# Kernel optimization log

Measured on AMD Instinct MI355X. Metric: run time of the kernel, lower is better.

Reference implementation:

```python
import jax, jax.numpy as jnp
import numpy as np

NUM_EMBEDDINGS = 512
EMBEDDING_DIM = 64
COMMITMENT_COST = 0.25


def setup_inputs() -> dict:
    key = jax.random.key(0)
    k1, k2 = jax.random.split(key)
    inputs = jax.random.normal(k1, (16, EMBEDDING_DIM, 4096), dtype=jnp.float32)
    # torch init: uniform(-1/num_embeddings, 1/num_embeddings)
    codebook = jax.random.uniform(
        k2, (NUM_EMBEDDINGS, EMBEDDING_DIM), dtype=jnp.float32,
        minval=-1.0 / NUM_EMBEDDINGS, maxval=1.0 / NUM_EMBEDDINGS)
    return {"inputs": inputs, "codebook": codebook}


def reference(inputs, codebook):
    # inputs: [B, D, T] -> permute to [B, T, D]
    x = jnp.transpose(inputs, (0, 2, 1))
    B, T, D = x.shape
    K = codebook.shape[0]
    flat = x.reshape(-1, D)  # [N, D]

    distances = (jnp.sum(flat * flat, axis=1, keepdims=True)
                 + jnp.sum(codebook * codebook, axis=1)
                 - 2.0 * flat @ codebook.T)  # [N, K]
    idx = jnp.argmin(distances, axis=1)  # [N]
    encodings = jax.nn.one_hot(idx, K, dtype=jnp.float32)  # [N, K]

    # direct gather == encodings @ codebook
    quantized = codebook[idx].reshape(B, T, D)

    e_latent_loss = jnp.mean((jax.lax.stop_gradient(quantized) - x) ** 2)
    q_latent_loss = jnp.mean((quantized - jax.lax.stop_gradient(x)) ** 2)
    loss = q_latent_loss + COMMITMENT_COST * e_latent_loss

    # straight-through estimator
    quantized_st = x + jax.lax.stop_gradient(quantized - x)

    avg_probs = jnp.mean(encodings, axis=0)
    perplexity = jnp.exp(-jnp.sum(avg_probs * jnp.log(avg_probs + 1e-10)))

    return (loss, jnp.transpose(quantized_st, (0, 2, 1)), perplexity, encodings)
```

## Files before the change

### kernel.cpp

```cpp
#include <hip/hip_runtime.h>

#define B_ 16
#define D_ 64
#define T_ 4096
#define K_ 512
#define N_ (B_*T_)
#define Q_ (B_*D_*T_)
#define ENC_OFF ((size_t)(2 + Q_))

#define WS_LOSS    0
#define WS_HIST    16
#define WS_NE      2064
#define WS_CBH     4608
#define WS_CBL     70144

typedef __bf16 bf16x8 __attribute__((ext_vector_type(8)));
typedef float  f32x4  __attribute__((ext_vector_type(4)));
typedef float  f32x2  __attribute__((ext_vector_type(2)));

__global__ __launch_bounds__(256) void k0_init(const float* __restrict__ cb,
                                               float* __restrict__ ne,
                                               int* __restrict__ hist,
                                               double* __restrict__ loss,
                                               bf16x8* __restrict__ cbh,
                                               bf16x8* __restrict__ cbl) {
    int bidx = blockIdx.x, tid = threadIdx.x;

    {
        int code = bidx * 32 + (tid >> 3), sl = tid & 7;
        float s = 0.f;
#pragma unroll
        for (int j = 0; j < 8; ++j) { float c = cb[code * 64 + sl * 8 + j]; s = fmaf(c, c, s); }
        s += __shfl_xor(s, 1); s += __shfl_xor(s, 2); s += __shfl_xor(s, 4);
        if (sl == 0) ne[code] = s;
    }
    if (bidx == 0) {
        hist[tid] = 0; hist[tid + 256] = 0;
        if (tid == 0) *loss = 0.0;
    }

    int e = bidx * 256 + tid;
    int ct = e >> 7, ks = (e >> 6) & 1, lane = e & 63;
    int code  = ct * 16 + (lane & 15);
    int dbase = ks * 32 + ((lane >> 4) << 3);
    bf16x8 h, l;
#pragma unroll
    for (int j = 0; j < 8; ++j) {
        float v = cb[code * 64 + dbase + j];
        __bf16 hv = (__bf16)v;
        __bf16 lv = (__bf16)(v - (float)hv);
        h[j] = hv; l[j] = lv;
    }
    cbh[(ct * 2 + ks) * 64 + lane] = h;
    cbl[(ct * 2 + ks) * 64 + lane] = l;
}

__global__ __launch_bounds__(256, 8) void k_main(const float* __restrict__ in,
                                                 const float* __restrict__ cb,
                                                 const bf16x8* __restrict__ cbh,
                                                 const bf16x8* __restrict__ cbl,
                                                 const float* __restrict__ ne,
                                                 float* __restrict__ out,
                                                 f32x2* __restrict__ enc2,
                                                 int* __restrict__ hist,
                                                 double* __restrict__ loss) {
    __shared__ float X[64][33];
    __shared__ float ne_s[512];
    __shared__ float smin[2][32];
    __shared__ int   smid[2][32];
    __shared__ int   sidx[32];
    int tid = threadIdx.x;
    int n0 = blockIdx.x * 32;
    int b  = n0 >> 12, t0 = n0 & (T_ - 1);

    {
        int d = tid >> 2, c0 = (tid & 3) * 8;
        const float4* ip = (const float4*)(in + ((size_t)b * 64 + d) * T_ + t0 + c0);
        float4 v0 = ip[0], v1 = ip[1];
        X[d][c0 + 0] = v0.x; X[d][c0 + 1] = v0.y; X[d][c0 + 2] = v0.z; X[d][c0 + 3] = v0.w;
        X[d][c0 + 4] = v1.x; X[d][c0 + 5] = v1.y; X[d][c0 + 6] = v1.z; X[d][c0 + 7] = v1.w;
    }
    ne_s[tid] = ne[tid];
    ne_s[tid + 256] = ne[tid + 256];
    __syncthreads();

    int w = tid >> 6, lane = tid & 63;
    int col = lane & 15, q = lane >> 4;
    int rt = w & 1;
    int ch = w >> 1;

    bf16x8 Ah[2], Al[2];
#pragma unroll
    for (int ks = 0; ks < 2; ++ks) {
        bf16x8 h, l;
#pragma unroll
        for (int j = 0; j < 8; ++j) {
            float v = X[ks * 32 + q * 8 + j][rt * 16 + col];
            __bf16 hv = (__bf16)v;
            __bf16 lv = (__bf16)(v - (float)hv);
            h[j] = hv; l[j] = lv;
        }
        Ah[ks] = h; Al[ks] = l;
    }

    float m1[4]; int i1[4];
#pragma unroll
    for (int e = 0; e < 4; ++e) { m1[e] = 3.4e38f; i1[e] = 0; }

    for (int c16 = 0; c16 < 16; ++c16) {
        int ct = ch * 16 + c16;
        bf16x8 Bh0 = cbh[(ct * 2 + 0) * 64 + lane];
        bf16x8 Bh1 = cbh[(ct * 2 + 1) * 64 + lane];
        bf16x8 Bl0 = cbl[(ct * 2 + 0) * 64 + lane];
        bf16x8 Bl1 = cbl[(ct * 2 + 1) * 64 + lane];
        float nev = ne_s[ct * 16 + col];
        int code = ct * 16 + col;
        f32x4 acc = {0.f, 0.f, 0.f, 0.f};
        acc = __builtin_amdgcn_mfma_f32_16x16x32_bf16(Ah[0], Bh0, acc, 0, 0, 0);
        acc = __builtin_amdgcn_mfma_f32_16x16x32_bf16(Ah[1], Bh1, acc, 0, 0, 0);
        acc = __builtin_amdgcn_mfma_f32_16x16x32_bf16(Ah[0], Bl0, acc, 0, 0, 0);
        acc = __builtin_amdgcn_mfma_f32_16x16x32_bf16(Al[0], Bh0, acc, 0, 0, 0);
        acc = __builtin_amdgcn_mfma_f32_16x16x32_bf16(Ah[1], Bl1, acc, 0, 0, 0);
        acc = __builtin_amdgcn_mfma_f32_16x16x32_bf16(Al[1], Bh1, acc, 0, 0, 0);
#pragma unroll
        for (int e = 0; e < 4; ++e) {
            float sc = fmaf(-2.f, acc[e], nev);
            bool lt = sc < m1[e];
            i1[e] = lt ? code : i1[e];
            m1[e] = lt ? sc : m1[e];
        }
    }

#pragma unroll
    for (int e = 0; e < 4; ++e) {
        float a1 = m1[e]; int ai = i1[e];
#pragma unroll
        for (int off = 1; off < 16; off <<= 1) {
            float o1 = __shfl_xor(a1, off);
            int   oi = __shfl_xor(ai, off);
            bool tk = (o1 < a1) || (o1 == a1 && oi < ai);
            a1 = tk ? o1 : a1; ai = tk ? oi : ai;
        }
        if (col == 0) { smin[ch][rt * 16 + q * 4 + e] = a1; smid[ch][rt * 16 + q * 4 + e] = ai; }
    }
    __syncthreads();

    if (tid < 32) {
        float a1 = smin[0][tid]; int ai = smid[0][tid];
        float o1 = smin[1][tid]; int oi = smid[1][tid];
        bool tk = (o1 < a1);
        sidx[tid] = tk ? oi : ai;
    }
    __syncthreads();

#pragma unroll 4
    for (int i = 0; i < 32; ++i) {
        int id = sidx[i];
        f32x2 v;
        v[0] = ((id >> 1) == tid && (id & 1) == 0) ? 1.f : 0.f;
        v[1] = ((id >> 1) == tid && (id & 1) == 1) ? 1.f : 0.f;
        enc2[(size_t)(n0 + i) * 256 + tid] = v;
    }

    int tl = tid & 31, dg = tid >> 5;
    int idq = sidx[tl];
    const float4* cq4 = (const float4*)(cb + (size_t)idq * 64 + dg * 8);
    float* qp = out + 1 + (size_t)b * D_ * T_ + (size_t)(dg * 8) * T_ + t0 + tl;

    float lsum = 0.f;
#pragma unroll
    for (int j4 = 0; j4 < 2; ++j4) {
        float4 qv = cq4[j4];
        float qe[4] = {qv.x, qv.y, qv.z, qv.w};
#pragma unroll
        for (int e = 0; e < 4; ++e) {
            int dl = j4 * 4 + e;
            float xv = X[dg * 8 + dl][tl];
            float diff = qe[e] - xv;
            lsum = fmaf(diff, diff, lsum);
            qp[(size_t)dl * T_] = xv + diff;
        }
    }
    if (tid < 32) atomicAdd(&hist[sidx[tid]], 1);

#pragma unroll
    for (int off = 32; off > 0; off >>= 1) lsum += __shfl_down(lsum, off);
    __shared__ float wsum[4];
    if ((tid & 63) == 0) wsum[tid >> 6] = lsum;
    __syncthreads();
    if (tid == 0) {
        double s = (double)wsum[0] + (double)wsum[1] + (double)wsum[2] + (double)wsum[3];
        atomicAdd(loss, s);
    }
}

__global__ __launch_bounds__(512) void k6_final(const int* __restrict__ hist,
                                                const double* __restrict__ loss,
                                                float* __restrict__ out) {
    __shared__ double sh[512];
    int k = threadIdx.x;
    double p = (double)hist[k] / (double)N_;
    sh[k] = p * log(p + 1e-10);
    __syncthreads();
    for (int s = 256; s > 0; s >>= 1) {
        if (k < s) sh[k] += sh[k + s];
        __syncthreads();
    }
    if (k == 0) {
        out[1 + Q_] = (float)exp(-sh[0]);
        out[0] = (float)(1.25 * (*loss) / (double)Q_);
    }
}

extern "C" void kernel_launch(void* const* d_in, const int* in_sizes, int n_in,
                              void* d_out, int out_size, void* d_ws, size_t ws_size,
                              hipStream_t stream) {
    const float* in = (const float*)d_in[0];
    const float* cb = (const float*)d_in[1];
    float* out = (float*)d_out;
    char* ws = (char*)d_ws;

    double* loss  = (double*)(ws + WS_LOSS);
    int* hist     = (int*)(ws + WS_HIST);
    float* ne     = (float*)(ws + WS_NE);
    bf16x8* cbh   = (bf16x8*)(ws + WS_CBH);
    bf16x8* cbl   = (bf16x8*)(ws + WS_CBL);

    f32x2* enc2 = (f32x2*)(out + ENC_OFF);

    k0_init<<<16, 256, 0, stream>>>(cb, ne, hist, loss, cbh, cbl);
    k_main<<<N_ / 32, 256, 0, stream>>>(in, cb, cbh, cbl, ne, out, enc2, hist, loss);
    k6_final<<<1, 512, 0, stream>>>(hist, loss, out);
}
```

Measured before the change: 202.5 us.

## Halve rows per block and split codebook across four waves

```diff
diff --git a/kernel.cpp b/kernel.cpp
--- a/kernel.cpp
+++ b/kernel.cpp
@@ -64,21 +64,20 @@
                                                  f32x2* __restrict__ enc2,
                                                  int* __restrict__ hist,
                                                  double* __restrict__ loss) {
-    __shared__ float X[64][33];
+    __shared__ float X[64][17];
     __shared__ float ne_s[512];
-    __shared__ float smin[2][32];
-    __shared__ int   smid[2][32];
-    __shared__ int   sidx[32];
+    __shared__ float smin[4][16];
+    __shared__ int   smid[4][16];
+    __shared__ int   sidx[16];
     int tid = threadIdx.x;
-    int n0 = blockIdx.x * 32;
+    int n0 = blockIdx.x * 16;
     int b  = n0 >> 12, t0 = n0 & (T_ - 1);
 
     {
-        int d = tid >> 2, c0 = (tid & 3) * 8;
-        const float4* ip = (const float4*)(in + ((size_t)b * 64 + d) * T_ + t0 + c0);
-        float4 v0 = ip[0], v1 = ip[1];
-        X[d][c0 + 0] = v0.x; X[d][c0 + 1] = v0.y; X[d][c0 + 2] = v0.z; X[d][c0 + 3] = v0.w;
-        X[d][c0 + 4] = v1.x; X[d][c0 + 5] = v1.y; X[d][c0 + 6] = v1.z; X[d][c0 + 7] = v1.w;
+        int d = tid >> 2, rg = (tid & 3) * 4;
+        const float4* ip = (const float4*)(in + ((size_t)b * 64 + d) * T_ + t0 + rg);
+        float4 v = ip[0];
+        X[d][rg + 0] = v.x; X[d][rg + 1] = v.y; X[d][rg + 2] = v.z; X[d][rg + 3] = v.w;
     }
     ne_s[tid] = ne[tid];
     ne_s[tid + 256] = ne[tid + 256];
@@ -86,8 +85,6 @@
 
     int w = tid >> 6, lane = tid & 63;
     int col = lane & 15, q = lane >> 4;
-    int rt = w & 1;
-    int ch = w >> 1;
 
     bf16x8 Ah[2], Al[2];
 #pragma unroll
@@ -95,7 +92,7 @@
         bf16x8 h, l;
 #pragma unroll
         for (int j = 0; j < 8; ++j) {
-            float v = X[ks * 32 + q * 8 + j][rt * 16 + col];
+            float v = X[ks * 32 + q * 8 + j][col];
             __bf16 hv = (__bf16)v;
             __bf16 lv = (__bf16)(v - (float)hv);
             h[j] = hv; l[j] = lv;
@@ -107,8 +104,8 @@
 #pragma unroll
     for (int e = 0; e < 4; ++e) { m1[e] = 3.4e38f; i1[e] = 0; }
 
-    for (int c16 = 0; c16 < 16; ++c16) {
-        int ct = ch * 16 + c16;
+    for (int c8 = 0; c8 < 8; ++c8) {
+        int ct = w * 8 + c8;
         bf16x8 Bh0 = cbh[(ct * 2 + 0) * 64 + lane];
         bf16x8 Bh1 = cbh[(ct * 2 + 1) * 64 + lane];
         bf16x8 Bl0 = cbl[(ct * 2 + 0) * 64 + lane];
@@ -141,47 +138,48 @@
             bool tk = (o1 < a1) || (o1 == a1 && oi < ai);
             a1 = tk ? o1 : a1; ai = tk ? oi : ai;
         }
-        if (col == 0) { smin[ch][rt * 16 + q * 4 + e] = a1; smid[ch][rt * 16 + q * 4 + e] = ai; }
-    }
-    __syncthreads();
-
-    if (tid < 32) {
+        if (col == 0) { smin[w][q * 4 + e] = a1; smid[w][q * 4 + e] = ai; }
+    }
+    __syncthreads();
+
+    if (tid < 16) {
         float a1 = smin[0][tid]; int ai = smid[0][tid];
-        float o1 = smin[1][tid]; int oi = smid[1][tid];
-        bool tk = (o1 < a1);
-        sidx[tid] = tk ? oi : ai;
+#pragma unroll
+        for (int w2 = 1; w2 < 4; ++w2) {
+            float o1 = smin[w2][tid]; int oi = smid[w2][tid];
+            bool tk = (o1 < a1);
+            a1 = tk ? o1 : a1; ai = tk ? oi : ai;
+        }
+        sidx[tid] = ai;
     }
     __syncthreads();
 
 #pragma unroll 4
-    for (int i = 0; i < 32; ++i) {
-        int id = sidx[i];
+    for (int i = 0; i < 16; ++i) {
+        int c = i * 256 + tid;
+        int row = c >> 8, k2 = c & 255;
+        int id = sidx[row];
         f32x2 v;
-        v[0] = ((id >> 1) == tid && (id & 1) == 0) ? 1.f : 0.f;
-        v[1] = ((id >> 1) == tid && (id & 1) == 1) ? 1.f : 0.f;
-        enc2[(size_t)(n0 + i) * 256 + tid] = v;
-    }
-
-    int tl = tid & 31, dg = tid >> 5;
-    int idq = sidx[tl];
-    const float4* cq4 = (const float4*)(cb + (size_t)idq * 64 + dg * 8);
-    float* qp = out + 1 + (size_t)b * D_ * T_ + (size_t)(dg * 8) * T_ + t0 + tl;
+        v[0] = (id == k2 * 2)     ? 1.f : 0.f;
+        v[1] = (id == k2 * 2 + 1) ? 1.f : 0.f;
+        enc2[(size_t)(n0 + row) * 256 + k2] = v;
+    }
+
+    int r = tid & 15, dg = tid >> 4;
+    int idq = sidx[r];
+    float4 qv = *(const float4*)(cb + (size_t)idq * 64 + dg * 4);
+    float qe[4] = {qv.x, qv.y, qv.z, qv.w};
+    float* qp = out + 1 + (size_t)b * D_ * T_ + (size_t)(dg * 4) * T_ + t0 + r;
 
     float lsum = 0.f;
 #pragma unroll
-    for (int j4 = 0; j4 < 2; ++j4) {
-        float4 qv = cq4[j4];
-        float qe[4] = {qv.x, qv.y, qv.z, qv.w};
-#pragma unroll
-        for (int e = 0; e < 4; ++e) {
-            int dl = j4 * 4 + e;
-            float xv = X[dg * 8 + dl][tl];
-            float diff = qe[e] - xv;
-            lsum = fmaf(diff, diff, lsum);
-            qp[(size_t)dl * T_] = xv + diff;
-        }
-    }
-    if (tid < 32) atomicAdd(&hist[sidx[tid]], 1);
+    for (int e = 0; e < 4; ++e) {
+        float xv = X[dg * 4 + e][r];
+        float diff = qe[e] - xv;
+        lsum = fmaf(diff, diff, lsum);
+        qp[(size_t)e * T_] = xv + diff;
+    }
+    if (tid < 16) atomicAdd(&hist[sidx[tid]], 1);
 
 #pragma unroll
     for (int off = 32; off > 0; off >>= 1) lsum += __shfl_down(lsum, off);
@@ -229,6 +227,6 @@
     f32x2* enc2 = (f32x2*)(out + ENC_OFF);
 
     k0_init<<<16, 256, 0, stream>>>(cb, ne, hist, loss, cbh, cbl);
-    k_main<<<N_ / 32, 256, 0, stream>>>(in, cb, cbh, cbl, ne, out, enc2, hist, loss);
+    k_main<<<N_ / 16, 256, 0, stream>>>(in, cb, cbh, cbl, ne, out, enc2, hist, loss);
     k6_final<<<1, 512, 0, stream>>>(hist, loss, out);
 }
```

Result: slower. 226.7 us (+12.0%).
